# Optimization experiments

Hardware: AMD Instinct MI355X
Metric: run time of the kernel (lower is better)

The kernel has to match this reference:

```python
import jax, jax.numpy as jnp
import numpy as np

# geomloss SamplesLoss(loss='sinkhorn', p=2, blur=0.05, scaling=0.8) constants
P = 2
BLUR = 0.05
SCALING = 0.8
# inputs are L2-normalized, so the point-cloud diameter is bounded by 2
DIAMETER = 2.0


def _eps_list():
    # geomloss epsilon_schedule: anneal eps from diameter**p down to blur**p
    e = [DIAMETER ** P]
    e += [float(np.exp(v)) for v in np.arange(P * np.log(DIAMETER), P * np.log(BLUR), P * np.log(SCALING))]
    e += [BLUR ** P]
    return e


def _cost(a, b):
    # geomloss p=2 cost: 0.5 * squared Euclidean distance, shape [N, M]
    sq = jnp.sum(a * a, -1)[:, None] + jnp.sum(b * b, -1)[None, :] - 2.0 * (a @ b.T)
    return 0.5 * jnp.maximum(sq, 0.0)


def _softmin(eps, C, h):
    # h = log-weights + potential/eps over the reduced axis; returns [N]
    return -eps * jax.nn.logsumexp(h[None, :] - C / eps, axis=1)


def _sinkhorn_divergence(x, y):
    # Debiased Sinkhorn divergence with epsilon-scaling (geomloss sinkhorn_tensorized)
    sg = jax.lax.stop_gradient
    N, M = x.shape[0], y.shape[0]
    a_log = jnp.full((N,), -np.log(N), x.dtype)  # uniform weights 1/N (log)
    b_log = jnp.full((M,), -np.log(M), y.dtype)

    C_xy = _cost(x, y)
    C_yx = C_xy.T
    C_xx = _cost(x, x)
    C_yy = _cost(y, y)
    # Sinkhorn loop runs without gradient (envelope theorem), like torch no_grad
    D_xy, D_yx, D_xx, D_yy = sg(C_xy), sg(C_yx), sg(C_xx), sg(C_yy)

    eps_list = _eps_list()
    eps = eps_list[0]
    g_ab = _softmin(eps, D_yx, a_log)   # potential on y for OT(a, b)
    f_ba = _softmin(eps, D_xy, b_log)   # potential on x for OT(a, b)
    f_aa = _softmin(eps, D_xx, a_log)   # debiasing potential OT(a, a)
    g_bb = _softmin(eps, D_yy, b_log)   # debiasing potential OT(b, b)

    for eps in eps_list:
        ft_ba = _softmin(eps, D_xy, b_log + g_ab / eps)
        gt_ab = _softmin(eps, D_yx, a_log + f_ba / eps)
        ft_aa = _softmin(eps, D_xx, a_log + f_aa / eps)
        gt_bb = _softmin(eps, D_yy, b_log + g_bb / eps)
        f_ba = 0.5 * (f_ba + ft_ba)
        g_ab = 0.5 * (g_ab + gt_ab)
        f_aa = 0.5 * (f_aa + ft_aa)
        g_bb = 0.5 * (g_bb + gt_bb)

    # final extrapolation with gradients enabled, dual potentials detached
    eps = eps_list[-1]
    f_ba, g_ab = (
        _softmin(eps, C_xy, sg(b_log + g_ab / eps)),
        _softmin(eps, C_yx, sg(a_log + f_ba / eps)),
    )
    f_aa = _softmin(eps, C_xx, sg(a_log + f_aa / eps))
    g_bb = _softmin(eps, C_yy, sg(b_log + g_bb / eps))

    # S_eps(a,b) = <a, f_ba - f_aa> + <b, g_ab - g_bb>, uniform weights
    return jnp.mean(f_ba - f_aa) + jnp.mean(g_ab - g_bb)


def setup_inputs() -> dict:
    key = jax.random.key(0)
    kx, ky = jax.random.split(key)
    x = jax.random.normal(kx, (4096, 64), jnp.float32)
    y = jax.random.normal(ky, (4096, 64), jnp.float32)
    return {"x": x, "y": y}


def reference(x, y):
    x = x / jnp.linalg.norm(x, axis=1, keepdims=True)
    y = y / jnp.linalg.norm(y, axis=1, keepdims=True)
    return _sinkhorn_divergence(x, y)
```

## Files before the change

### kernel.cpp

```cpp
#include <hip/hip_runtime.h>
#include <math.h>

#define NPTS 4096
#define DIM 64
#define NM ((size_t)NPTS * (size_t)NPTS)
#define LOGW (-8.317766166719343f)
#define NEGINF (-__builtin_inff())

typedef __bf16 bf16x8 __attribute__((ext_vector_type(8)));
typedef float f32x4 __attribute__((ext_vector_type(4)));
typedef _Float16 half8 __attribute__((ext_vector_type(8)));

static __device__ __forceinline__ f32x4 mfma16(bf16x8 a, bf16x8 b, f32x4 c) {
  return __builtin_amdgcn_mfma_f32_16x16x32_bf16(a, b, c, 0, 0, 0);
}

__global__ __launch_bounds__(256) void norm_split_kernel(
    const float* __restrict__ x, const float* __restrict__ y,
    __bf16* __restrict__ xh, __bf16* __restrict__ xl,
    __bf16* __restrict__ yh, __bf16* __restrict__ yl) {
  int row  = blockIdx.x * 4 + (threadIdx.x >> 6);
  int lane = threadIdx.x & 63;
  const float* src; __bf16 *dh, *dl;
  if (row < NPTS) {
    src = x + (size_t)row * DIM; dh = xh + (size_t)row * DIM; dl = xl + (size_t)row * DIM;
  } else {
    int r = row - NPTS;
    src = y + (size_t)r * DIM; dh = yh + (size_t)r * DIM; dl = yl + (size_t)r * DIM;
  }
  float v = src[lane];
  float s = v * v;
  #pragma unroll
  for (int o = 32; o; o >>= 1) s += __shfl_xor(s, o, 64);
  v *= 1.0f / sqrtf(s);
  __bf16 h = (__bf16)v;
  __bf16 l = (__bf16)(v - (float)h);
  dh[lane] = h;
  dl[lane] = l;
}

__global__ __launch_bounds__(256) void cost_mfma_kernel(
    const __bf16* __restrict__ xh, const __bf16* __restrict__ xl,
    const __bf16* __restrict__ yh, const __bf16* __restrict__ yl,
    _Float16* __restrict__ Cw) {
  int mat = blockIdx.z;
  const __bf16 *Ah, *Al, *Bh, *Bl;
  if (mat == 0)      { Ah = xh; Al = xl; Bh = yh; Bl = yl; }
  else if (mat == 1) { Ah = yh; Al = yl; Bh = xh; Bl = xl; }
  else if (mat == 2) { Ah = xh; Al = xl; Bh = xh; Bl = xl; }
  else               { Ah = yh; Al = yl; Bh = yh; Bl = yl; }
  _Float16* Cout = Cw + (size_t)mat * NM;

  int i0 = blockIdx.y * 64, j0 = blockIdx.x * 64;
  int wave = threadIdx.x >> 6, L = threadIdx.x & 63;
  int mrow = L & 15, quad = L >> 4;

  size_t abase = (size_t)(i0 + wave * 16 + mrow) * DIM + quad * 8;
  bf16x8 ah0 = *(const bf16x8*)(Ah + abase);
  bf16x8 ah1 = *(const bf16x8*)(Ah + abase + 32);
  bf16x8 al0 = *(const bf16x8*)(Al + abase);
  bf16x8 al1 = *(const bf16x8*)(Al + abase + 32);

  #pragma unroll
  for (int ct = 0; ct < 4; ++ct) {
    size_t bbase = (size_t)(j0 + ct * 16 + mrow) * DIM + quad * 8;
    bf16x8 bh0 = *(const bf16x8*)(Bh + bbase);
    bf16x8 bh1 = *(const bf16x8*)(Bh + bbase + 32);
    bf16x8 bl0 = *(const bf16x8*)(Bl + bbase);
    bf16x8 bl1 = *(const bf16x8*)(Bl + bbase + 32);
    f32x4 acc = {0.0f, 0.0f, 0.0f, 0.0f};
    acc = mfma16(ah0, bh0, acc);
    acc = mfma16(ah1, bh1, acc);
    acc = mfma16(al0, bh0, acc);
    acc = mfma16(al1, bh1, acc);
    acc = mfma16(ah0, bl0, acc);
    acc = mfma16(ah1, bl1, acc);
    int gj = j0 + ct * 16 + mrow;
    #pragma unroll
    for (int q = 0; q < 4; ++q) {
      int gi = i0 + wave * 16 + quad * 4 + q;
      Cout[(size_t)gi * NPTS + gj] = (_Float16)fmaxf(1.0f - acc[q], 0.0f);
    }
  }
}

__global__ __launch_bounds__(256) void pass_kernel(
    const _Float16* __restrict__ Cw,
    const float* __restrict__ potOld, float* __restrict__ potNew,
    float inv_eps, float eps, int use_pot, int avg) {
  int blk  = blockIdx.x;
  int mat  = blk >> 10;
  int row  = (blk & 1023) * 4 + (threadIdx.x >> 6);
  int lane = threadIdx.x & 63;
  const _Float16* Crow = Cw + (size_t)mat * NM + (size_t)row * NPTS;
  int ridx = (mat == 0) ? 1 : ((mat == 1) ? 0 : mat);
  const float* pot = potOld + (size_t)ridx * NPTS;

  float m0 = NEGINF, s0 = 0.0f, m1 = NEGINF, s1 = 0.0f;
  #pragma unroll 2
  for (int t = 0; t < 8; ++t) {
    int j = lane * 8 + t * 512;
    half8 c8 = *(const half8*)(Crow + j);
    float h[8];
    if (use_pot) {
      float4 pa = *(const float4*)(pot + j);
      float4 pb = *(const float4*)(pot + j + 4);
      h[0] = fmaf(pa.x, inv_eps, LOGW); h[1] = fmaf(pa.y, inv_eps, LOGW);
      h[2] = fmaf(pa.z, inv_eps, LOGW); h[3] = fmaf(pa.w, inv_eps, LOGW);
      h[4] = fmaf(pb.x, inv_eps, LOGW); h[5] = fmaf(pb.y, inv_eps, LOGW);
      h[6] = fmaf(pb.z, inv_eps, LOGW); h[7] = fmaf(pb.w, inv_eps, LOGW);
    } else {
      #pragma unroll
      for (int e = 0; e < 8; ++e) h[e] = LOGW;
    }
    #pragma unroll
    for (int e = 0; e < 8; e += 2) {
      float tv = fmaf((float)c8[e], -inv_eps, h[e]);
      float mn = fmaxf(m0, tv);
      s0 = s0 * __expf(m0 - mn) + __expf(tv - mn);
      m0 = mn;
      float tv1 = fmaf((float)c8[e + 1], -inv_eps, h[e + 1]);
      float mn1 = fmaxf(m1, tv1);
      s1 = s1 * __expf(m1 - mn1) + __expf(tv1 - mn1);
      m1 = mn1;
    }
  }
  {
    float mn = fmaxf(m0, m1);
    s0 = s0 * __expf(m0 - mn) + s1 * __expf(m1 - mn);
    m0 = mn;
  }
  #pragma unroll
  for (int o = 1; o < 64; o <<= 1) {
    float m2 = __shfl_xor(m0, o, 64);
    float s2 = __shfl_xor(s0, o, 64);
    float mn = fmaxf(m0, m2);
    s0 = s0 * __expf(m0 - mn) + s2 * __expf(m2 - mn);
    m0 = mn;
  }
  if (lane == 0) {
    float ft = -eps * (m0 + __logf(s0));
    float v = avg ? 0.5f * (potOld[(size_t)mat * NPTS + row] + ft) : ft;
    potNew[(size_t)mat * NPTS + row] = v;
  }
}

__global__ __launch_bounds__(256) void final_kernel(
    const float* __restrict__ pot, float* __restrict__ out) {
  __shared__ float red[256];
  float s = 0.0f;
  for (int j = threadIdx.x; j < NPTS; j += 256)
    s += (pot[j] - pot[2 * NPTS + j]) + (pot[NPTS + j] - pot[3 * NPTS + j]);
  red[threadIdx.x] = s;
  __syncthreads();
  #pragma unroll
  for (int o = 128; o; o >>= 1) {
    if (threadIdx.x < o) red[threadIdx.x] += red[threadIdx.x + o];
    __syncthreads();
  }
  if (threadIdx.x == 0) out[0] = red[0] / (float)NPTS;
}

extern "C" void kernel_launch(void* const* d_in, const int* in_sizes, int n_in,
                              void* d_out, int out_size, void* d_ws, size_t ws_size,
                              hipStream_t stream) {
  const float* x = (const float*)d_in[0];
  const float* y = (const float*)d_in[1];
  char* ws = (char*)d_ws;

  _Float16* Cw = (_Float16*)ws;
  __bf16* xh = (__bf16*)(ws + 4 * NM * sizeof(_Float16));
  __bf16* xl = xh + (size_t)NPTS * DIM;
  __bf16* yh = xl + (size_t)NPTS * DIM;
  __bf16* yl = yh + (size_t)NPTS * DIM;
  float* potA = (float*)(yl + (size_t)NPTS * DIM);
  float* potB = potA + 4 * (size_t)NPTS;
  size_t needed = (size_t)((char*)(potB + 4 * (size_t)NPTS) - ws);
  if (ws_size < needed) return;

  norm_split_kernel<<<2048, 256, 0, stream>>>(x, y, xh, xl, yh, yl);
  cost_mfma_kernel<<<dim3(64, 64, 4), 256, 0, stream>>>(xh, xl, yh, yl, Cw);

  double lst[32];
  int c = 0;
  lst[c++] = 4.0;
  double start = 2.0 * log(2.0), stop = 2.0 * log(0.05), step = 2.0 * log(0.8);
  for (int k = 0;; ++k) {
    double v = start + (double)k * step;
    if (v <= stop) break;
    lst[c++] = exp(v);
  }
  lst[c++] = 0.05 * 0.05;

  for (int p = 0; p < c + 2; ++p) {
    double e = (p == 0) ? lst[0] : ((p <= c) ? lst[p - 1] : lst[c - 1]);
    float eps = (float)e;
    float inv_eps = 1.0f / eps;
    int use_pot = (p > 0) ? 1 : 0;
    int avg = (p >= 1 && p <= c) ? 1 : 0;
    const float* po = (p & 1) ? potB : potA;
    float* pn       = (p & 1) ? potA : potB;
    pass_kernel<<<4096, 256, 0, stream>>>(Cw, po, pn, inv_eps, eps, use_pot, avg);
  }
  final_kernel<<<1, 256, 0, stream>>>(potB, (float*)d_out);
}
```

Baseline: 818.1 us.

## Fuse cost-matrix computation into each Sinkhorn pass instead of materializing fp16 costs

```diff
diff --git a/kernel.cpp b/kernel.cpp
--- a/kernel.cpp
+++ b/kernel.cpp
@@ -3,13 +3,11 @@
 
 #define NPTS 4096
 #define DIM 64
-#define NM ((size_t)NPTS * (size_t)NPTS)
 #define LOGW (-8.317766166719343f)
 #define NEGINF (-__builtin_inff())
 
 typedef __bf16 bf16x8 __attribute__((ext_vector_type(8)));
 typedef float f32x4 __attribute__((ext_vector_type(4)));
-typedef _Float16 half8 __attribute__((ext_vector_type(8)));
 
 static __device__ __forceinline__ f32x4 mfma16(bf16x8 a, bf16x8 b, f32x4 c) {
   return __builtin_amdgcn_mfma_f32_16x16x32_bf16(a, b, c, 0, 0, 0);
@@ -39,110 +37,119 @@
   dl[lane] = l;
 }
 
-__global__ __launch_bounds__(256) void cost_mfma_kernel(
+__global__ __launch_bounds__(256) void pass_kernel(
     const __bf16* __restrict__ xh, const __bf16* __restrict__ xl,
     const __bf16* __restrict__ yh, const __bf16* __restrict__ yl,
-    _Float16* __restrict__ Cw) {
+    const float* __restrict__ potOld, float2* __restrict__ part,
+    float inv_eps, int use_pot) {
   int mat = blockIdx.z;
   const __bf16 *Ah, *Al, *Bh, *Bl;
   if (mat == 0)      { Ah = xh; Al = xl; Bh = yh; Bl = yl; }
   else if (mat == 1) { Ah = yh; Al = yl; Bh = xh; Bl = xl; }
   else if (mat == 2) { Ah = xh; Al = xl; Bh = xh; Bl = xl; }
   else               { Ah = yh; Al = yl; Bh = yh; Bl = yl; }
-  _Float16* Cout = Cw + (size_t)mat * NM;
-
-  int i0 = blockIdx.y * 64, j0 = blockIdx.x * 64;
+  int ridx = (mat == 0) ? 1 : ((mat == 1) ? 0 : mat);
+
+  int colbase = blockIdx.x * 512;
+  __shared__ float hp[512];
+  {
+    int t0 = threadIdx.x;
+    #pragma unroll
+    for (int e = 0; e < 2; ++e) {
+      int jj = t0 + e * 256;
+      float p = use_pot ? potOld[(size_t)ridx * NPTS + colbase + jj] : 0.0f;
+      hp[jj] = fmaf(p, inv_eps, LOGW) - inv_eps;
+    }
+  }
+  __syncthreads();
+
   int wave = threadIdx.x >> 6, L = threadIdx.x & 63;
   int mrow = L & 15, quad = L >> 4;
-
-  size_t abase = (size_t)(i0 + wave * 16 + mrow) * DIM + quad * 8;
-  bf16x8 ah0 = *(const bf16x8*)(Ah + abase);
-  bf16x8 ah1 = *(const bf16x8*)(Ah + abase + 32);
-  bf16x8 al0 = *(const bf16x8*)(Al + abase);
-  bf16x8 al1 = *(const bf16x8*)(Al + abase + 32);
-
-  #pragma unroll
-  for (int ct = 0; ct < 4; ++ct) {
-    size_t bbase = (size_t)(j0 + ct * 16 + mrow) * DIM + quad * 8;
-    bf16x8 bh0 = *(const bf16x8*)(Bh + bbase);
-    bf16x8 bh1 = *(const bf16x8*)(Bh + bbase + 32);
-    bf16x8 bl0 = *(const bf16x8*)(Bl + bbase);
-    bf16x8 bl1 = *(const bf16x8*)(Bl + bbase + 32);
-    f32x4 acc = {0.0f, 0.0f, 0.0f, 0.0f};
-    acc = mfma16(ah0, bh0, acc);
-    acc = mfma16(ah1, bh1, acc);
-    acc = mfma16(al0, bh0, acc);
-    acc = mfma16(al1, bh1, acc);
-    acc = mfma16(ah0, bl0, acc);
-    acc = mfma16(ah1, bl1, acc);
-    int gj = j0 + ct * 16 + mrow;
-    #pragma unroll
-    for (int q = 0; q < 4; ++q) {
-      int gi = i0 + wave * 16 + quad * 4 + q;
-      Cout[(size_t)gi * NPTS + gj] = (_Float16)fmaxf(1.0f - acc[q], 0.0f);
+  int row0 = blockIdx.y * 128 + wave * 32;
+
+  bf16x8 a_h[2][2], a_l[2][2];
+  #pragma unroll
+  for (int s = 0; s < 2; ++s) {
+    size_t ab = (size_t)(row0 + s * 16 + mrow) * DIM + quad * 8;
+    a_h[s][0] = *(const bf16x8*)(Ah + ab);
+    a_h[s][1] = *(const bf16x8*)(Ah + ab + 32);
+    a_l[s][0] = *(const bf16x8*)(Al + ab);
+    a_l[s][1] = *(const bf16x8*)(Al + ab + 32);
+  }
+
+  float m[2][4], sm[2][4];
+  #pragma unroll
+  for (int s = 0; s < 2; ++s)
+    #pragma unroll
+    for (int q = 0; q < 4; ++q) { m[s][q] = NEGINF; sm[s][q] = 0.0f; }
+
+  #pragma unroll 2
+  for (int ct = 0; ct < 32; ++ct) {
+    size_t bb = (size_t)(colbase + ct * 16 + mrow) * DIM + quad * 8;
+    bf16x8 bh0 = *(const bf16x8*)(Bh + bb);
+    bf16x8 bh1 = *(const bf16x8*)(Bh + bb + 32);
+    bf16x8 bl0 = *(const bf16x8*)(Bl + bb);
+    bf16x8 bl1 = *(const bf16x8*)(Bl + bb + 32);
+    float hpv = hp[ct * 16 + mrow];
+    #pragma unroll
+    for (int s = 0; s < 2; ++s) {
+      f32x4 acc = {0.0f, 0.0f, 0.0f, 0.0f};
+      acc = mfma16(a_h[s][0], bh0, acc);
+      acc = mfma16(a_h[s][1], bh1, acc);
+      acc = mfma16(a_l[s][0], bh0, acc);
+      acc = mfma16(a_l[s][1], bh1, acc);
+      acc = mfma16(a_h[s][0], bl0, acc);
+      acc = mfma16(a_h[s][1], bl1, acc);
+      #pragma unroll
+      for (int q = 0; q < 4; ++q) {
+        float t = fmaf(acc[q], inv_eps, hpv);
+        float mn = fmaxf(m[s][q], t);
+        sm[s][q] = fmaf(sm[s][q], __expf(m[s][q] - mn), __expf(t - mn));
+        m[s][q] = mn;
+      }
     }
   }
-}
-
-__global__ __launch_bounds__(256) void pass_kernel(
-    const _Float16* __restrict__ Cw,
+
+  #pragma unroll
+  for (int o = 1; o < 16; o <<= 1) {
+    #pragma unroll
+    for (int s = 0; s < 2; ++s)
+      #pragma unroll
+      for (int q = 0; q < 4; ++q) {
+        float m2 = __shfl_xor(m[s][q], o, 64);
+        float s2 = __shfl_xor(sm[s][q], o, 64);
+        float mn = fmaxf(m[s][q], m2);
+        sm[s][q] = sm[s][q] * __expf(m[s][q] - mn) + s2 * __expf(m2 - mn);
+        m[s][q] = mn;
+      }
+  }
+  if (mrow == 0) {
+    #pragma unroll
+    for (int s = 0; s < 2; ++s)
+      #pragma unroll
+      for (int q = 0; q < 4; ++q) {
+        int row = row0 + s * 16 + quad * 4 + q;
+        part[((size_t)mat * NPTS + row) * 8 + blockIdx.x] =
+            make_float2(m[s][q], sm[s][q]);
+      }
+  }
+}
+
+__global__ __launch_bounds__(256) void merge_kernel(
+    const float2* __restrict__ part,
     const float* __restrict__ potOld, float* __restrict__ potNew,
-    float inv_eps, float eps, int use_pot, int avg) {
-  int blk  = blockIdx.x;
-  int mat  = blk >> 10;
-  int row  = (blk & 1023) * 4 + (threadIdx.x >> 6);
-  int lane = threadIdx.x & 63;
-  const _Float16* Crow = Cw + (size_t)mat * NM + (size_t)row * NPTS;
-  int ridx = (mat == 0) ? 1 : ((mat == 1) ? 0 : mat);
-  const float* pot = potOld + (size_t)ridx * NPTS;
-
-  float m0 = NEGINF, s0 = 0.0f, m1 = NEGINF, s1 = 0.0f;
-  #pragma unroll 2
-  for (int t = 0; t < 8; ++t) {
-    int j = lane * 8 + t * 512;
-    half8 c8 = *(const half8*)(Crow + j);
-    float h[8];
-    if (use_pot) {
-      float4 pa = *(const float4*)(pot + j);
-      float4 pb = *(const float4*)(pot + j + 4);
-      h[0] = fmaf(pa.x, inv_eps, LOGW); h[1] = fmaf(pa.y, inv_eps, LOGW);
-      h[2] = fmaf(pa.z, inv_eps, LOGW); h[3] = fmaf(pa.w, inv_eps, LOGW);
-      h[4] = fmaf(pb.x, inv_eps, LOGW); h[5] = fmaf(pb.y, inv_eps, LOGW);
-      h[6] = fmaf(pb.z, inv_eps, LOGW); h[7] = fmaf(pb.w, inv_eps, LOGW);
-    } else {
-      #pragma unroll
-      for (int e = 0; e < 8; ++e) h[e] = LOGW;
-    }
-    #pragma unroll
-    for (int e = 0; e < 8; e += 2) {
-      float tv = fmaf((float)c8[e], -inv_eps, h[e]);
-      float mn = fmaxf(m0, tv);
-      s0 = s0 * __expf(m0 - mn) + __expf(tv - mn);
-      m0 = mn;
-      float tv1 = fmaf((float)c8[e + 1], -inv_eps, h[e + 1]);
-      float mn1 = fmaxf(m1, tv1);
-      s1 = s1 * __expf(m1 - mn1) + __expf(tv1 - mn1);
-      m1 = mn1;
-    }
-  }
-  {
-    float mn = fmaxf(m0, m1);
-    s0 = s0 * __expf(m0 - mn) + s1 * __expf(m1 - mn);
-    m0 = mn;
-  }
-  #pragma unroll
-  for (int o = 1; o < 64; o <<= 1) {
-    float m2 = __shfl_xor(m0, o, 64);
-    float s2 = __shfl_xor(s0, o, 64);
-    float mn = fmaxf(m0, m2);
-    s0 = s0 * __expf(m0 - mn) + s2 * __expf(m2 - mn);
-    m0 = mn;
-  }
-  if (lane == 0) {
-    float ft = -eps * (m0 + __logf(s0));
-    float v = avg ? 0.5f * (potOld[(size_t)mat * NPTS + row] + ft) : ft;
-    potNew[(size_t)mat * NPTS + row] = v;
-  }
+    float eps, int avg) {
+  int r = blockIdx.x * 256 + threadIdx.x;
+  float m = NEGINF, s = 0.0f;
+  #pragma unroll
+  for (int c = 0; c < 8; ++c) {
+    float2 p = part[(size_t)r * 8 + c];
+    float mn = fmaxf(m, p.x);
+    s = s * __expf(m - mn) + p.y * __expf(p.x - mn);
+    m = mn;
+  }
+  float ft = -eps * (m + __logf(s));
+  potNew[r] = avg ? 0.5f * (potOld[r] + ft) : ft;
 }
 
 __global__ __launch_bounds__(256) void final_kernel(
@@ -168,18 +175,17 @@
   const float* y = (const float*)d_in[1];
   char* ws = (char*)d_ws;
 
-  _Float16* Cw = (_Float16*)ws;
-  __bf16* xh = (__bf16*)(ws + 4 * NM * sizeof(_Float16));
+  __bf16* xh = (__bf16*)ws;
   __bf16* xl = xh + (size_t)NPTS * DIM;
   __bf16* yh = xl + (size_t)NPTS * DIM;
   __bf16* yl = yh + (size_t)NPTS * DIM;
   float* potA = (float*)(yl + (size_t)NPTS * DIM);
   float* potB = potA + 4 * (size_t)NPTS;
-  size_t needed = (size_t)((char*)(potB + 4 * (size_t)NPTS) - ws);
+  float2* part = (float2*)(potB + 4 * (size_t)NPTS);
+  size_t needed = (size_t)((char*)(part + 4 * (size_t)NPTS * 8) - ws);
   if (ws_size < needed) return;
 
   norm_split_kernel<<<2048, 256, 0, stream>>>(x, y, xh, xl, yh, yl);
-  cost_mfma_kernel<<<dim3(64, 64, 4), 256, 0, stream>>>(xh, xl, yh, yl, Cw);
 
   double lst[32];
   int c = 0;
@@ -200,7 +206,9 @@
     int avg = (p >= 1 && p <= c) ? 1 : 0;
     const float* po = (p & 1) ? potB : potA;
     float* pn       = (p & 1) ? potA : potB;
-    pass_kernel<<<4096, 256, 0, stream>>>(Cw, po, pn, inv_eps, eps, use_pot, avg);
+    pass_kernel<<<dim3(8, 32, 4), 256, 0, stream>>>(
+        xh, xl, yh, yl, po, part, inv_eps, use_pot);
+    merge_kernel<<<64, 256, 0, stream>>>(part, po, pn, eps, avg);
   }
   final_kernel<<<1, 256, 0, stream>>>(potB, (float*)d_out);
 }
```

New measurement: 1.488 ms. +81.9%, slower.
